# Performance work log

Measured on AMD Instinct MI355X. Metric: run time of the kernel, lower is better.

## Reference

```python
import jax, jax.numpy as jnp
import numpy as np
from jax import lax

IN_DIM, OUT_DIM, GROUPS, K, DEGREE, PAD = 64, 128, 4, 3, 3, 1
IN_G = IN_DIM // GROUPS    # 16
OUT_G = OUT_DIM // GROUPS  # 32
EPS = 1e-5


def setup_inputs() -> dict:
    key = jax.random.key(0)
    k1, k2 = jax.random.split(key)
    x = jax.random.normal(k1, (64, IN_DIM, 64, 64), jnp.float32)
    # meta (hypernetwork-generated) weight: (out_g, in_g*(degree+2), k, k)
    layer_weight = jax.random.normal(k2, (OUT_G, IN_G * (DEGREE + 2), K, K), jnp.float32) * 0.05
    return {"x": x, "layer_weight": layer_weight}


def _conv(x, w):
    # plain NCHW conv2d, groups=1, stride=1, dilation=1, symmetric padding
    return lax.conv_general_dilated(
        x, w, window_strides=(1, 1), padding=[(PAD, PAD), (PAD, PAD)],
        dimension_numbers=("NCHW", "OIHW", "NCHW"))


def _legendre_basis(x, order):
    # recursive Legendre polynomials P0..P_order, concatenated on channel dim
    polys = [jnp.ones_like(x), x]
    for n in range(1, order):
        pn = ((2.0 * n + 1.0) * x * polys[-1] - n * polys[-2]) / (n + 1.0)
        polys.append(pn)
    return jnp.concatenate(polys, axis=1)  # [B, in_g*(order+1), H, W]


def _group_forward(xg, w):
    # xg: [B, in_g, H, W]; w: [out_g, in_g*(degree+2), k, k]
    base_w = w[:, :IN_G]                                   # (out_g, in_g, k, k)
    base_out = _conv(jax.nn.silu(xg), base_w)
    # global min-max normalization over the whole group tensor
    xmin, xmax = xg.min(), xg.max()
    x_norm = 2.0 * (xg - xmin) / (xmax - xmin) - 1.0
    lb = _legendre_basis(x_norm, DEGREE)                   # [B, in_g*(degree+1), H, W]
    poly_w = w[:, IN_G:].reshape(OUT_G, IN_G * (DEGREE + 1), K, K)
    y = base_out + _conv(lb, poly_w)
    # InstanceNorm2d (affine=False, no running stats): per-sample per-channel
    mean = y.mean(axis=(2, 3), keepdims=True)
    var = y.var(axis=(2, 3), keepdims=True)
    y = (y - mean) * lax.rsqrt(var + EPS)
    return jax.nn.silu(y)


def reference(x, layer_weight):
    B, C, H, W = x.shape
    # split channels into groups, vmap over groups (same weight for each group)
    xg = x.reshape(B, GROUPS, IN_G, H, W).transpose(1, 0, 2, 3, 4)  # [G,B,in_g,H,W]
    yg = jax.vmap(lambda xx: _group_forward(xx, layer_weight))(xg)  # [G,B,out_g,H,W]
    return yg.transpose(1, 0, 2, 3, 4).reshape(B, OUT_DIM, H, W)
```

## Files before the change

kernel.cpp:

```cpp
#include <hip/hip_runtime.h>
#include <hip/hip_bf16.h>


#define NB 64
#define NH 64
#define NW 64

typedef __attribute__((ext_vector_type(8)))  short bf16x8;
typedef __attribute__((ext_vector_type(16))) float f32x16;

#define WLDS_BYTES 36864
#define AUG_BYTES  41472
#define TL_BYTES   1152
#define SMEM_BYTES (WLDS_BYTES + AUG_BYTES + TL_BYTES)

__device__ __forceinline__ float silu(float v) {
    return v / (1.0f + __expf(-v));
}
__device__ __forceinline__ unsigned short tobf(float f) {
    union { __hip_bfloat16 h; unsigned short u; } cv;
    cv.h = __float2bfloat16(f);
    return cv.u;
}

__global__ __launch_bounds__(256) void minmax_kernel(const float* __restrict__ x,
                                                     float* __restrict__ pmm) {
    int plane = blockIdx.x;
    const float4* p = (const float4*)(x + (size_t)plane * 4096);
    int t = threadIdx.x;
    float mn = 3.4e38f, mx = -3.4e38f;
    #pragma unroll
    for (int k = 0; k < 4; ++k) {
        float4 v = p[t + k * 256];
        mn = fminf(mn, fminf(fminf(v.x, v.y), fminf(v.z, v.w)));
        mx = fmaxf(mx, fmaxf(fmaxf(v.x, v.y), fmaxf(v.z, v.w)));
    }
    #pragma unroll
    for (int off = 32; off; off >>= 1) {
        mn = fminf(mn, __shfl_xor(mn, off));
        mx = fmaxf(mx, __shfl_xor(mx, off));
    }
    __shared__ float smn[4], smx[4];
    int wid = t >> 6, lane = t & 63;
    if (lane == 0) { smn[wid] = mn; smx[wid] = mx; }
    __syncthreads();
    if (t == 0) {
        mn = fminf(fminf(smn[0], smn[1]), fminf(smn[2], smn[3]));
        mx = fmaxf(fmaxf(smx[0], smx[1]), fmaxf(smx[2], smx[3]));
        pmm[plane * 2]     = mn;
        pmm[plane * 2 + 1] = mx;
    }
}

__global__ __launch_bounds__(256) void reduce_repack_kernel(const float* __restrict__ pmm,
                                                            const float* __restrict__ w,
                                                            float* __restrict__ wsf,
                                                            unsigned short* __restrict__ wpk,
                                                            float* __restrict__ Tt) {
    int blk = blockIdx.x;
    int t = threadIdx.x;
    if (blk < 4) {
        int g = blk;
        float mn = 3.4e38f, mx = -3.4e38f;
        #pragma unroll
        for (int j = 0; j < 4; ++j) {
            int p = t + j * 256;
            int b = p >> 4, c = p & 15;
            int plane = b * 64 + g * 16 + c;
            mn = fminf(mn, pmm[plane * 2]);
            mx = fmaxf(mx, pmm[plane * 2 + 1]);
        }
        #pragma unroll
        for (int off = 32; off; off >>= 1) {
            mn = fminf(mn, __shfl_xor(mn, off));
            mx = fmaxf(mx, __shfl_xor(mx, off));
        }
        __shared__ float smn[4], smx[4];
        int wid = t >> 6, lane = t & 63;
        if (lane == 0) { smn[wid] = mn; smx[wid] = mx; }
        __syncthreads();
        if (t == 0) {
            mn = fminf(fminf(smn[0], smn[1]), fminf(smn[2], smn[3]));
            mx = fmaxf(fmaxf(smx[0], smx[1]), fmaxf(smx[2], smx[3]));
            wsf[g * 2]     = mn;
            wsf[g * 2 + 1] = mx;
        }
    } else if (blk < 76) {
        int idx = (blk - 4) * 256 + t;
        int tap = idx / 2048;
        int r   = idx - tap * 2048;
        int kq  = r >> 8;
        int oc  = (r >> 3) & 31;
        int j   = r & 7;
        int k   = kq * 8 + j;
        int orig = (k < 16) ? k : (k + 16);
        wpk[idx] = tobf(w[oc * 720 + orig * 9 + tap]);
    } else {
        for (int i = t; i < 288; i += 256) {
            int oc = i / 9, ty = i - oc * 9;
            int ey = ty / 3, ex = ty - ey * 3;
            int ky0 = (ey == 0) ? 1 : 0, ky1 = (ey == 2) ? 1 : 2;
            int kx0 = (ex == 0) ? 1 : 0, kx1 = (ex == 2) ? 1 : 2;
            float s = 0.f;
            for (int c = 0; c < 16; ++c)
                for (int ky = ky0; ky <= ky1; ++ky)
                    for (int kx = kx0; kx <= kx1; ++kx)
                        s += w[oc * 720 + (16 + c) * 9 + ky * 3 + kx];
            Tt[i] = s;
        }
    }
}

__global__ __launch_bounds__(512, 4) void conv_mfma_kernel(const float* __restrict__ x,
                                                           const float* __restrict__ wsf,
                                                           const unsigned short* __restrict__ wpk,
                                                           const float* __restrict__ Tt,
                                                           float* __restrict__ out) {
    extern __shared__ char smem[];
    unsigned short* wl  = (unsigned short*)smem;
    unsigned short* aug = (unsigned short*)(smem + WLDS_BYTES);
    float*          Tl  = (float*)(smem + WLDS_BYTES + AUG_BYTES);

    int flat = blockIdx.x;
    int f = ((flat & 7) << 9) | (flat >> 3);
    int tile = f & 15;
    int bg = f >> 4;
    int b = bg & 63;
    int g = bg >> 6;
    int th0 = (tile >> 2) * 16, tw0 = (tile & 3) * 16;

    float xmin = wsf[g * 2];
    float xmax = wsf[g * 2 + 1];
    float inv = 2.0f / (xmax - xmin);

    const float* xg = x + ((size_t)b * 64 + g * 16) * 4096;
    int t = threadIdx.x;

    {
        const uint4* src = (const uint4*)wpk;
        uint4* dst = (uint4*)wl;
        #pragma unroll
        for (int i = 0; i < 5; ++i) {
            int idx = t + i * 512;
            if (idx < 2304) dst[idx] = src[idx];
        }
    }
    if (t < 288) Tl[t] = Tt[t];

    #pragma unroll
    for (int i = 0; i < 3; ++i) {
        int idx = t + i * 512;
        if (idx < 1296) {
            int kind = idx / 324;
            int pix = idx - kind * 324;
            int ly = pix / 18, lx = pix - ly * 18;
            int gh = th0 + ly - 1, gw = tw0 + lx - 1;
            bool ok = (gh >= 0 && gh < NH && gw >= 0 && gw < NW);
            const float* src = xg + gh * 64 + gw;
            if (kind < 2) {
                int c0 = kind * 8;
                bf16x8 v;
                #pragma unroll
                for (int j = 0; j < 8; ++j) {
                    float val = ok ? src[(size_t)(c0 + j) * 4096] : 0.f;
                    v[j] = (short)tobf(silu(val));
                }
                *(bf16x8*)&aug[(kind * 324 + pix) * 8] = v;
            } else {
                int half = kind & 1;
                int c0 = half * 8;
                bf16x8 v1, v2, v3;
                #pragma unroll
                for (int j = 0; j < 8; ++j) {
                    float val = ok ? src[(size_t)(c0 + j) * 4096] : 0.f;
                    float xn = (val - xmin) * inv - 1.f;
                    float p2 = 1.5f * xn * xn - 0.5f;
                    float p3 = (2.5f * xn * xn - 1.5f) * xn;
                    v1[j] = ok ? (short)tobf(xn) : (short)0;
                    v2[j] = ok ? (short)tobf(p2) : (short)0;
                    v3[j] = ok ? (short)tobf(p3) : (short)0;
                }
                *(bf16x8*)&aug[((2 + half) * 324 + pix) * 8] = v1;
                *(bf16x8*)&aug[((4 + half) * 324 + pix) * 8] = v2;
                *(bf16x8*)&aug[((6 + half) * 324 + pix) * 8] = v3;
            }
        }
    }
    __syncthreads();

    int wv = t >> 6;
    int lane = t & 63;
    int lo = lane & 31, hi = lane >> 5;
    int py = 2 * wv + (lo >> 4), px = lo & 15;

    f32x16 acc = {};
    #pragma unroll
    for (int tap = 0; tap < 9; ++tap) {
        const int ky = tap / 3, kx = tap % 3;
        const int hp = (py + ky) * 18 + (px + kx);
        #pragma unroll
        for (int kcg = 0; kcg < 4; ++kcg) {
            bf16x8 Af = *(const bf16x8*)&wl[((tap * 8 + kcg * 2 + hi) * 32 + lo) * 8];
            bf16x8 Bf = *(const bf16x8*)&aug[(((kcg * 2 + hi) * 324) + hp) * 8];
            acc = __builtin_amdgcn_mfma_f32_32x32x16_bf16(Af, Bf, acc, 0, 0, 0);
        }
    }

    int h = th0 + py, wc = tw0 + px;
    int ey = (h == 0) ? 0 : ((h == NH - 1) ? 2 : 1);
    int ex = (wc == 0) ? 0 : ((wc == NW - 1) ? 2 : 1);
    int et = ey * 3 + ex;
    size_t obase = ((size_t)b * 128 + g * 32) * 4096 + (size_t)h * 64 + wc;
    #pragma unroll
    for (int r = 0; r < 16; ++r) {
        int oc = (r & 3) + 8 * (r >> 2) + 4 * hi;
        out[obase + (size_t)oc * 4096] = acc[r] + Tl[oc * 9 + et];
    }
}

__global__ __launch_bounds__(256) void norm_kernel(float* __restrict__ out) {
    int plane = blockIdx.x;
    float4* p = (float4*)(out + (size_t)plane * 4096);
    int t = threadIdx.x;
    float4 v[4];
    float s = 0.f, s2 = 0.f;
    #pragma unroll
    for (int k = 0; k < 4; ++k) {
        v[k] = p[t + k * 256];
        s  += v[k].x + v[k].y + v[k].z + v[k].w;
        s2 += v[k].x * v[k].x + v[k].y * v[k].y + v[k].z * v[k].z + v[k].w * v[k].w;
    }
    #pragma unroll
    for (int off = 32; off; off >>= 1) {
        s  += __shfl_xor(s, off);
        s2 += __shfl_xor(s2, off);
    }
    __shared__ float ss[4], ss2[4];
    int wid = t >> 6, lane = t & 63;
    if (lane == 0) { ss[wid] = s; ss2[wid] = s2; }
    __syncthreads();
    s  = ss[0] + ss[1] + ss[2] + ss[3];
    s2 = ss2[0] + ss2[1] + ss2[2] + ss2[3];
    float mean = s * (1.f / 4096.f);
    float var  = fmaxf(s2 * (1.f / 4096.f) - mean * mean, 0.f);
    float istd = rsqrtf(var + 1e-5f);
    #pragma unroll
    for (int k = 0; k < 4; ++k) {
        float4 o;
        o.x = (v[k].x - mean) * istd; o.x = silu(o.x);
        o.y = (v[k].y - mean) * istd; o.y = silu(o.y);
        o.z = (v[k].z - mean) * istd; o.z = silu(o.z);
        o.w = (v[k].w - mean) * istd; o.w = silu(o.w);
        p[t + k * 256] = o;
    }
}

extern "C" void kernel_launch(void* const* d_in, const int* in_sizes, int n_in,
                              void* d_out, int out_size, void* d_ws, size_t ws_size,
                              hipStream_t stream) {
    const float* x = (const float*)d_in[0];
    const float* w = (const float*)d_in[1];
    float* out = (float*)d_out;
    float* wsf = (float*)d_ws;
    float* pmm = (float*)((char*)d_ws + 64);
    unsigned short* wpk = (unsigned short*)((char*)d_ws + 64 + 32768);
    float* Tt = (float*)((char*)d_ws + 64 + 32768 + 36864);

    static int smem_set = 0;
    if (!smem_set) {
        hipFuncSetAttribute((const void*)conv_mfma_kernel,
                            hipFuncAttributeMaxDynamicSharedMemorySize, SMEM_BYTES);
        smem_set = 1;
    }

    hipLaunchKernelGGL(minmax_kernel, dim3(NB * 64), dim3(256), 0, stream, x, pmm);
    hipLaunchKernelGGL(reduce_repack_kernel, dim3(77), dim3(256), 0, stream, pmm, w, wsf, wpk, Tt);
    hipLaunchKernelGGL(conv_mfma_kernel, dim3(4096), dim3(512), SMEM_BYTES, stream, x, wsf, wpk, Tt, out);
    hipLaunchKernelGGL(norm_kernel, dim3(NB * 128), dim3(256), 0, stream, out);
}
```

Measured before the change: 148.7 us.

## Make conv kernel persistent per (batch,group) with double-buffered tile staging

The conv kernel now launches one block per (batch, group) instead of per 16x16 tile. Each block loads the packed weights into LDS once and loops over 16 spatial tiles, prefetching the next tile's inputs into registers while running the MFMAs on the current LDS buffer. Each thread now computes silu and the Legendre terms for a pixel from a single load, instead of two threads loading the same input. The MFMA chain is split into two accumulators. In exchange, the grid shrinks from 4096 to 256 blocks, and the doubled LDS cuts occupancy to 2 blocks per CU, which may leave CUs underused.

New measurement: 180.7 us. 1.21x slower.

```diff
diff --git a/kernel.cpp b/kernel.cpp
--- a/kernel.cpp
+++ b/kernel.cpp
@@ -12,7 +12,7 @@
 #define WLDS_BYTES 36864
 #define AUG_BYTES  41472
 #define TL_BYTES   1152
-#define SMEM_BYTES (WLDS_BYTES + AUG_BYTES + TL_BYTES)
+#define SMEM_BYTES (WLDS_BYTES + 2 * AUG_BYTES + TL_BYTES)
 
 __device__ __forceinline__ float silu(float v) {
     return v / (1.0f + __expf(-v));
@@ -111,23 +111,70 @@
     }
 }
 
-__global__ __launch_bounds__(512, 4) void conv_mfma_kernel(const float* __restrict__ x,
+__device__ __forceinline__ void stage_load(const float* __restrict__ xg, int tile,
+                                           int t, float r[2][8], bool okv[2]) {
+    int th0 = (tile >> 2) * 16, tw0 = (tile & 3) * 16;
+    #pragma unroll
+    for (int i = 0; i < 2; ++i) {
+        int idx = t + i * 512;
+        if (idx < 648) {
+            int half = idx >= 324 ? 1 : 0;
+            int pix = idx - half * 324;
+            int ly = pix / 18, lx = pix - ly * 18;
+            int gh = th0 + ly - 1, gw = tw0 + lx - 1;
+            bool ok = (gh >= 0 && gh < NH && gw >= 0 && gw < NW);
+            okv[i] = ok;
+            const float* s = xg + (size_t)(half * 8) * 4096 + gh * 64 + gw;
+            #pragma unroll
+            for (int j = 0; j < 8; ++j)
+                r[i][j] = ok ? s[(size_t)j * 4096] : 0.f;
+        }
+    }
+}
+
+__device__ __forceinline__ void stage_write(unsigned short* __restrict__ buf, int t,
+                                            const float r[2][8], const bool okv[2],
+                                            float xmin, float inv) {
+    #pragma unroll
+    for (int i = 0; i < 2; ++i) {
+        int idx = t + i * 512;
+        if (idx < 648) {
+            int half = idx >= 324 ? 1 : 0;
+            int pix = idx - half * 324;
+            bool ok = okv[i];
+            bf16x8 vs, v1, v2, v3;
+            #pragma unroll
+            for (int j = 0; j < 8; ++j) {
+                float val = r[i][j];
+                vs[j] = (short)tobf(silu(val));
+                float xn = (val - xmin) * inv - 1.f;
+                float p2 = 1.5f * xn * xn - 0.5f;
+                float p3 = (2.5f * xn * xn - 1.5f) * xn;
+                v1[j] = ok ? (short)tobf(xn) : (short)0;
+                v2[j] = ok ? (short)tobf(p2) : (short)0;
+                v3[j] = ok ? (short)tobf(p3) : (short)0;
+            }
+            *(bf16x8*)&buf[((0 + half) * 324 + pix) * 8] = vs;
+            *(bf16x8*)&buf[((2 + half) * 324 + pix) * 8] = v1;
+            *(bf16x8*)&buf[((4 + half) * 324 + pix) * 8] = v2;
+            *(bf16x8*)&buf[((6 + half) * 324 + pix) * 8] = v3;
+        }
+    }
+}
+
+__global__ __launch_bounds__(512, 2) void conv_mfma_kernel(const float* __restrict__ x,
                                                            const float* __restrict__ wsf,
                                                            const unsigned short* __restrict__ wpk,
                                                            const float* __restrict__ Tt,
                                                            float* __restrict__ out) {
     extern __shared__ char smem[];
-    unsigned short* wl  = (unsigned short*)smem;
-    unsigned short* aug = (unsigned short*)(smem + WLDS_BYTES);
-    float*          Tl  = (float*)(smem + WLDS_BYTES + AUG_BYTES);
-
-    int flat = blockIdx.x;
-    int f = ((flat & 7) << 9) | (flat >> 3);
-    int tile = f & 15;
-    int bg = f >> 4;
-    int b = bg & 63;
-    int g = bg >> 6;
-    int th0 = (tile >> 2) * 16, tw0 = (tile & 3) * 16;
+    unsigned short* wl   = (unsigned short*)smem;
+    unsigned short* augA = (unsigned short*)(smem + WLDS_BYTES);
+    unsigned short* augB = (unsigned short*)(smem + WLDS_BYTES + AUG_BYTES);
+    float*          Tl   = (float*)(smem + WLDS_BYTES + 2 * AUG_BYTES);
+
+    int f = blockIdx.x;
+    int b = f >> 2, g = f & 3;
 
     float xmin = wsf[g * 2];
     float xmax = wsf[g * 2 + 1];
@@ -146,75 +193,59 @@
         }
     }
     if (t < 288) Tl[t] = Tt[t];
-
-    #pragma unroll
-    for (int i = 0; i < 3; ++i) {
-        int idx = t + i * 512;
-        if (idx < 1296) {
-            int kind = idx / 324;
-            int pix = idx - kind * 324;
-            int ly = pix / 18, lx = pix - ly * 18;
-            int gh = th0 + ly - 1, gw = tw0 + lx - 1;
-            bool ok = (gh >= 0 && gh < NH && gw >= 0 && gw < NW);
-            const float* src = xg + gh * 64 + gw;
-            if (kind < 2) {
-                int c0 = kind * 8;
-                bf16x8 v;
-                #pragma unroll
-                for (int j = 0; j < 8; ++j) {
-                    float val = ok ? src[(size_t)(c0 + j) * 4096] : 0.f;
-                    v[j] = (short)tobf(silu(val));
-                }
-                *(bf16x8*)&aug[(kind * 324 + pix) * 8] = v;
-            } else {
-                int half = kind & 1;
-                int c0 = half * 8;
-                bf16x8 v1, v2, v3;
-                #pragma unroll
-                for (int j = 0; j < 8; ++j) {
-                    float val = ok ? src[(size_t)(c0 + j) * 4096] : 0.f;
-                    float xn = (val - xmin) * inv - 1.f;
-                    float p2 = 1.5f * xn * xn - 0.5f;
-                    float p3 = (2.5f * xn * xn - 1.5f) * xn;
-                    v1[j] = ok ? (short)tobf(xn) : (short)0;
-                    v2[j] = ok ? (short)tobf(p2) : (short)0;
-                    v3[j] = ok ? (short)tobf(p3) : (short)0;
-                }
-                *(bf16x8*)&aug[((2 + half) * 324 + pix) * 8] = v1;
-                *(bf16x8*)&aug[((4 + half) * 324 + pix) * 8] = v2;
-                *(bf16x8*)&aug[((6 + half) * 324 + pix) * 8] = v3;
-            }
-        }
-    }
-    __syncthreads();
 
     int wv = t >> 6;
     int lane = t & 63;
     int lo = lane & 31, hi = lane >> 5;
     int py = 2 * wv + (lo >> 4), px = lo & 15;
 
-    f32x16 acc = {};
-    #pragma unroll
-    for (int tap = 0; tap < 9; ++tap) {
-        const int ky = tap / 3, kx = tap % 3;
-        const int hp = (py + ky) * 18 + (px + kx);
-        #pragma unroll
-        for (int kcg = 0; kcg < 4; ++kcg) {
-            bf16x8 Af = *(const bf16x8*)&wl[((tap * 8 + kcg * 2 + hi) * 32 + lo) * 8];
-            bf16x8 Bf = *(const bf16x8*)&aug[(((kcg * 2 + hi) * 324) + hp) * 8];
-            acc = __builtin_amdgcn_mfma_f32_32x32x16_bf16(Af, Bf, acc, 0, 0, 0);
-        }
-    }
-
-    int h = th0 + py, wc = tw0 + px;
-    int ey = (h == 0) ? 0 : ((h == NH - 1) ? 2 : 1);
-    int ex = (wc == 0) ? 0 : ((wc == NW - 1) ? 2 : 1);
-    int et = ey * 3 + ex;
-    size_t obase = ((size_t)b * 128 + g * 32) * 4096 + (size_t)h * 64 + wc;
-    #pragma unroll
-    for (int r = 0; r < 16; ++r) {
-        int oc = (r & 3) + 8 * (r >> 2) + 4 * hi;
-        out[obase + (size_t)oc * 4096] = acc[r] + Tl[oc * 9 + et];
+    {
+        float r[2][8]; bool okv[2];
+        stage_load(xg, 0, t, r, okv);
+        stage_write(augA, t, r, okv, xmin, inv);
+    }
+    __syncthreads();
+
+    size_t gbase = ((size_t)b * 128 + g * 32) * 4096;
+
+    for (int tile = 0; tile < 16; ++tile) {
+        unsigned short* cur = (tile & 1) ? augB : augA;
+        unsigned short* nxt = (tile & 1) ? augA : augB;
+
+        float r[2][8]; bool okv[2];
+        if (tile < 15) stage_load(xg, tile + 1, t, r, okv);
+
+        f32x16 acc0 = {}, acc1 = {};
+        #pragma unroll
+        for (int tap = 0; tap < 9; ++tap) {
+            const int ky = tap / 3, kx = tap % 3;
+            const int hp = (py + ky) * 18 + (px + kx);
+            #pragma unroll
+            for (int kcg = 0; kcg < 4; ++kcg) {
+                bf16x8 Af = *(const bf16x8*)&wl[((tap * 8 + kcg * 2 + hi) * 32 + lo) * 8];
+                bf16x8 Bf = *(const bf16x8*)&cur[(((kcg * 2 + hi) * 324) + hp) * 8];
+                if (tap & 1)
+                    acc1 = __builtin_amdgcn_mfma_f32_32x32x16_bf16(Af, Bf, acc1, 0, 0, 0);
+                else
+                    acc0 = __builtin_amdgcn_mfma_f32_32x32x16_bf16(Af, Bf, acc0, 0, 0, 0);
+            }
+        }
+
+        if (tile < 15) stage_write(nxt, t, r, okv, xmin, inv);
+
+        int th0 = (tile >> 2) * 16, tw0 = (tile & 3) * 16;
+        int h = th0 + py, wc = tw0 + px;
+        int ey = (h == 0) ? 0 : ((h == NH - 1) ? 2 : 1);
+        int ex = (wc == 0) ? 0 : ((wc == NW - 1) ? 2 : 1);
+        int et = ey * 3 + ex;
+        size_t obase = gbase + (size_t)h * 64 + wc;
+        #pragma unroll
+        for (int rr = 0; rr < 16; ++rr) {
+            int oc = (rr & 3) + 8 * (rr >> 2) + 4 * hi;
+            out[obase + (size_t)oc * 4096] = acc0[rr] + acc1[rr] + Tl[oc * 9 + et];
+        }
+
+        __syncthreads();
     }
 }
 
@@ -275,6 +306,6 @@
 
     hipLaunchKernelGGL(minmax_kernel, dim3(NB * 64), dim3(256), 0, stream, x, pmm);
     hipLaunchKernelGGL(reduce_repack_kernel, dim3(77), dim3(256), 0, stream, pmm, w, wsf, wpk, Tt);
-    hipLaunchKernelGGL(conv_mfma_kernel, dim3(4096), dim3(512), SMEM_BYTES, stream, x, wsf, wpk, Tt, out);
+    hipLaunchKernelGGL(conv_mfma_kernel, dim3(256), dim3(512), SMEM_BYTES, stream, x, wsf, wpk, Tt, out);
     hipLaunchKernelGGL(norm_kernel, dim3(NB * 128), dim3(256), 0, stream, out);
 }
```
